# Kernel tuning notes

Measured on AMD Instinct MI355X. Metric: run time of the kernel, lower is better.

Reference implementation:

```python
import jax, jax.numpy as jnp
import numpy as np

B, T_ENC, T_DEC = 16, 256, 200
E, ATT, PRE, H, MEL, LOC, K = 512, 128, 256, 1024, 80, 32, 31


def setup_inputs() -> dict:
    key = jax.random.key(0)
    ks = jax.random.split(key, 20)
    s = lambda k, shape: jax.random.normal(k, shape, jnp.float32) * 0.02
    return dict(
        encoder_output=jax.random.normal(ks[0], (B, T_ENC, E), jnp.float32),
        padded_mels=jax.random.normal(ks[1], (B, T_DEC, MEL), jnp.float32),
        enc_proj_w=s(ks[2], (ATT, E)),
        lstm_proj_w=s(ks[3], (ATT, H)),
        loc_conv_w=s(ks[4], (LOC, 1, K)),
        loc_conv_b=jnp.zeros((LOC,), jnp.float32),
        loc_dense_w=s(ks[5], (ATT, LOC)),
        loc_dense_b=jnp.zeros((ATT,), jnp.float32),
        e_w=s(ks[6], (1, ATT)),
        e_b=jnp.zeros((1,), jnp.float32),
        prenet1_w=s(ks[7], (PRE, MEL)),
        prenet2_w=s(ks[8], (PRE, PRE)),
        w_ih0=s(ks[9], (4 * H, PRE + E)),
        w_hh0=s(ks[10], (4 * H, H)),
        b_ih0=jnp.zeros((4 * H,), jnp.float32),
        b_hh0=jnp.zeros((4 * H,), jnp.float32),
        w_ih1=s(ks[11], (4 * H, H)),
        w_hh1=s(ks[12], (4 * H, H)),
        b_ih1=jnp.zeros((4 * H,), jnp.float32),
        b_hh1=jnp.zeros((4 * H,), jnp.float32),
        proj_w=s(ks[13], (MEL, H + E)),
        proj_b=jnp.zeros((MEL,), jnp.float32),
        stop_w=s(ks[14], (1, H + E)),
        stop_b=jnp.zeros((1,), jnp.float32),
        text_lengths=jax.random.randint(ks[15], (B,), T_ENC // 2, T_ENC + 1),
    )


def _lstm_cell_zero(x, w_ih, b_ih, b_hh):
    # PyTorch LSTM cell with zero initial (h, c): h_prev contributes nothing
    # except the recurrent bias b_hh. Gate order: i, f, g, o.
    g = x @ w_ih.T + b_ih + b_hh
    i, f, gg, o = jnp.split(g, 4, axis=-1)
    c = jax.nn.sigmoid(i) * jnp.tanh(gg)  # f * c_prev == 0
    return jax.nn.sigmoid(o) * jnp.tanh(c)


def reference(encoder_output, padded_mels, enc_proj_w, lstm_proj_w, loc_conv_w,
              loc_conv_b, loc_dense_w, loc_dense_b, e_w, e_b, prenet1_w,
              prenet2_w, w_ih0, w_hh0, b_ih0, b_hh0, w_ih1, w_hh1, b_ih1,
              b_hh1, proj_w, proj_b, stop_w, stop_b, text_lengths):
    b, t_enc, _ = encoder_output.shape
    n_mel = padded_mels.shape[-1]
    h = w_hh0.shape[-1]
    pad = (loc_conv_w.shape[-1] - 1) // 2
    proc_enc = encoder_output @ enc_proj_w.T              # [B,Te,128]
    mask = jnp.arange(t_enc)[None, :] < text_lengths[:, None]
    # teacher forcing (ratio=1.0): prev mel at step t is padded_mels[:, t-1]
    prev_mels = jnp.concatenate(
        [jnp.zeros((b, 1, n_mel), padded_mels.dtype), padded_mels[:, :-1]],
        axis=1).transpose(1, 0, 2)                        # [Td,B,80]

    def step(carry, prev_mel):
        awc, h2 = carry                                   # [B,Te], [B,1024]
        # prenet (dropout omitted for a deterministic reference)
        x = jax.nn.relu(prev_mel @ prenet1_w.T)
        x = jax.nn.relu(x @ prenet2_w.T)                  # [B,256]
        # location-sensitive attention
        q = h2 @ lstm_proj_w.T                            # [B,128]
        loc = jax.lax.conv_general_dilated(
            awc[:, None, :], loc_conv_w, (1,), [(pad, pad)],
            dimension_numbers=('NCH', 'OIH', 'NCH')) + loc_conv_b[None, :, None]
        loc = jnp.einsum('bct,ac->bta', loc, loc_dense_w) + loc_dense_b
        en = jnp.tanh(q[:, None, :] + loc + proc_enc) @ e_w[0] + e_b[0]
        en = jnp.where(mask, en, -1e9)
        aw = jax.nn.softmax(en, axis=-1)                  # [B,Te]
        ctx = jnp.einsum('bt,bte->be', aw, encoder_output)  # [B,512]
        # 2-layer LSTM, state reset to zero every step (as in the original)
        li = jnp.concatenate([x, ctx], axis=-1)           # [B,768]
        h1 = _lstm_cell_zero(li, w_ih0, b_ih0, b_hh0)
        h2n = _lstm_cell_zero(h1, w_ih1, b_ih1, b_hh1)
        dec = jnp.concatenate([h2n, ctx], axis=-1)        # [B,1536]
        mel = dec @ proj_w.T + proj_b                     # [B,80]
        stop = (dec @ stop_w.T + stop_b)[:, 0]            # [B]
        return (awc + aw, h2n), (mel, stop)

    init = (jnp.zeros((b, t_enc), encoder_output.dtype),
            jnp.zeros((b, h), encoder_output.dtype))
    _, (mels, stops) = jax.lax.scan(step, init, prev_mels)
    return mels.transpose(1, 0, 2), stops.T               # [B,Td,80], [B,Td]
```

## Files before the change

kernel.cpp:

```cpp
#include <hip/hip_runtime.h>
#include <math.h>

#define NB   16
#define TE   256
#define TD   200
#define EE   512
#define ATT  128
#define PREN 256
#define HH   1024
#define NMEL 80
#define NLOC 32
#define KWW  31
#define PADW 15

#define OFF_X2H  0
#define OFF_PE   (OFF_X2H + TD*NB*128)
#define OFF_EN   (OFF_PE + NB*TE*ATT)
#define OFF_CTH  (OFF_EN + NB*TE)
#define OFF_H1H  (OFF_CTH + NB*256)
#define OFF_H2R  (OFF_H1H + NB*512)
#define OFF_QVR  (OFF_H2R + NB*256*4)
#define OFF_BAR  (OFF_QVR + NB*16*2*4)
#define BAR_U32  8192
#define ARR_G 0
#define ARR_L 4096

#define LW0X_U32 (12*128)
#define LW0C_U32 (12*256)
#define LW1_U32  (12*512)
#define DYN_BYTES ((LW0X_U32 + LW0C_U32 + LW1_U32)*4)

typedef float f4 __attribute__((ext_vector_type(4)));
typedef unsigned int u32x4 __attribute__((ext_vector_type(4)));
typedef unsigned int u32x2 __attribute__((ext_vector_type(2)));
typedef _Float16 h2t __attribute__((ext_vector_type(2)));

__device__ __forceinline__ float sigmf(float x) { return 1.0f / (1.0f + expf(-x)); }
__device__ __forceinline__ float dot4(f4 a, f4 b) {
  return a.x*b.x + a.y*b.y + a.z*b.z + a.w*b.w;
}
__device__ __forceinline__ float red32(float v) {
  v += __shfl_down(v, 16, 32); v += __shfl_down(v, 8, 32);
  v += __shfl_down(v, 4, 32);  v += __shfl_down(v, 2, 32);
  v += __shfl_down(v, 1, 32);
  return v;
}
__device__ __forceinline__ float red64(float v) {
  v += __shfl_down(v, 32); v += __shfl_down(v, 16); v += __shfl_down(v, 8);
  v += __shfl_down(v, 4);  v += __shfl_down(v, 2);  v += __shfl_down(v, 1);
  return v;
}
__device__ __forceinline__ float fdot2(unsigned a, unsigned b, float c) {
  return __builtin_amdgcn_fdot2(__builtin_bit_cast(h2t, a),
                                __builtin_bit_cast(h2t, b), c, false);
}
__device__ __forceinline__ unsigned pkh(float a, float b) {
  h2t h; h.x = (_Float16)a; h.y = (_Float16)b;
  return __builtin_bit_cast(unsigned, h);
}
__device__ __forceinline__ float hlo(unsigned u) {
  return (float)__builtin_bit_cast(h2t, u).x;
}
__device__ __forceinline__ float hhi(unsigned u) {
  return (float)__builtin_bit_cast(h2t, u).y;
}

__device__ __forceinline__ unsigned ld_cg_u32(const unsigned* p) {
  unsigned r;
  asm volatile("global_load_dword %0, %1, off sc0 sc1\n\ts_waitcnt vmcnt(0)"
               : "=v"(r) : "v"(p) : "memory");
  return r;
}
__device__ __forceinline__ void st_cg_u32(unsigned* p, unsigned v) {
  asm volatile("global_store_dword %0, %1, off sc0 sc1" :: "v"(p), "v"(v) : "memory");
}
__device__ __forceinline__ float ld_cg_f32(const float* p) {
  float r;
  asm volatile("global_load_dword %0, %1, off sc0 sc1\n\ts_waitcnt vmcnt(0)"
               : "=v"(r) : "v"(p) : "memory");
  return r;
}
__device__ __forceinline__ void st_cg_f32(float* p, float v) {
  asm volatile("global_store_dword %0, %1, off sc0 sc1" :: "v"(p), "v"(v) : "memory");
}
__device__ __forceinline__ f4 ld_cg_f4(const f4* p) {
  f4 r;
  asm volatile("global_load_dwordx4 %0, %1, off sc0 sc1\n\ts_waitcnt vmcnt(0)"
               : "=v"(r) : "v"(p) : "memory");
  return r;
}
__device__ __forceinline__ void st_cg_f4(f4* p, f4 v) {
  asm volatile("global_store_dwordx4 %0, %1, off sc0 sc1" :: "v"(p), "v"(v) : "memory");
}
__device__ __forceinline__ u32x4 ld_cg_u4(const void* p) {
  u32x4 r;
  asm volatile("global_load_dwordx4 %0, %1, off sc0 sc1\n\ts_waitcnt vmcnt(0)"
               : "=v"(r) : "v"(p) : "memory");
  return r;
}
__device__ __forceinline__ void st_cg_u2(void* p, u32x2 v) {
  asm volatile("global_store_dwordx2 %0, %1, off sc0 sc1" :: "v"(p), "v"(v) : "memory");
}
__device__ __forceinline__ void ld2u(u32x4& a, u32x4& b, const void* pa, const void* pb) {
  asm volatile(
    "global_load_dwordx4 %0, %2, off sc0 sc1\n\t"
    "global_load_dwordx4 %1, %3, off sc0 sc1\n\t"
    "s_waitcnt vmcnt(0)"
    : "=&v"(a), "=&v"(b) : "v"(pa), "v"(pb) : "memory");
}
__device__ __forceinline__ void ld4u(u32x4& a, u32x4& b, u32x4& c, u32x4& d,
                                     const void* pa, const void* pb,
                                     const void* pc, const void* pd) {
  asm volatile(
    "global_load_dwordx4 %0, %4, off sc0 sc1\n\t"
    "global_load_dwordx4 %1, %5, off sc0 sc1\n\t"
    "global_load_dwordx4 %2, %6, off sc0 sc1\n\t"
    "global_load_dwordx4 %3, %7, off sc0 sc1\n\t"
    "s_waitcnt vmcnt(0)"
    : "=&v"(a), "=&v"(b), "=&v"(c), "=&v"(d)
    : "v"(pa), "v"(pb), "v"(pc), "v"(pd) : "memory");
}

__device__ __forceinline__ void g_arrive(unsigned* bar, unsigned e) {
  __syncthreads();
  if (threadIdx.x == 0) st_cg_u32(bar + ARR_G + blockIdx.x * 16, e);
}
__device__ __forceinline__ void g_wait(unsigned* bar, unsigned e) {
  if (threadIdx.x < 256) {
    while (ld_cg_u32(bar + ARR_G + threadIdx.x * 16) < e) {}
  }
  __syncthreads();
}
__device__ __forceinline__ void l_arrive(unsigned* bar, unsigned e) {
  __syncthreads();
  if (threadIdx.x == 0) st_cg_u32(bar + ARR_L + blockIdx.x * 16, e);
}
__device__ __forceinline__ void l_wait(unsigned* bar, unsigned e, int b_grp) {
  if (threadIdx.x < 16) {
    while (ld_cg_u32(bar + ARR_L + (threadIdx.x * 16 + b_grp) * 16) < e) {}
  }
  __syncthreads();
}

__global__ void k_init(float* __restrict__ ws) {
  const int gid = blockIdx.x * 256 + threadIdx.x;
  f4* h2r = (f4*)(ws + OFF_H2R);
  f4* qvr = (f4*)(ws + OFF_QVR);
  unsigned* bar = (unsigned*)(ws + OFF_BAR);
  const f4 z = (f4){0.f, 0.f, 0.f, 0.f};
  for (int i = gid; i < NB*256; i += 32*256) st_cg_f4(h2r + i, z);
  for (int i = gid; i < NB*16*2; i += 32*256) st_cg_f4(qvr + i, z);
  for (int i = gid; i < BAR_U32; i += 32*256) st_cg_u32(bar + i, 0u);
}

__global__ void k_prenet(const float* __restrict__ mels,
                         const float* __restrict__ w1,
                         const float* __restrict__ w2,
                         float* __restrict__ ws) {
  const int t = blockIdx.x >> 4;
  const int b = blockIdx.x & 15;
  const int j = threadIdx.x;
  __shared__ float s_in[NMEL];
  __shared__ float s_x1[PREN];
  if (j < NMEL) s_in[j] = (t == 0) ? 0.0f : mels[(b*TD + (t-1))*NMEL + j];
  __syncthreads();
  float a1 = 0.0f;
  #pragma unroll 8
  for (int k = 0; k < NMEL; ++k) a1 += s_in[k] * w1[j*NMEL + k];
  s_x1[j] = fmaxf(a1, 0.0f);
  __syncthreads();
  float a2 = 0.0f;
  #pragma unroll 8
  for (int k = 0; k < PREN; ++k) a2 += s_x1[k] * w2[j*PREN + k];
  ((_Float16*)(ws + OFF_X2H))[((size_t)t*NB + b)*256 + j] = (_Float16)fmaxf(a2, 0.0f);
}

__global__ void k_procenc(const float* __restrict__ enc,
                          const float* __restrict__ w,
                          float* __restrict__ pe) {
  const int bt = blockIdx.x;
  const int a = threadIdx.x;
  __shared__ float s_e[EE];
  for (int k = a; k < EE; k += 128) s_e[k] = enc[bt*EE + k];
  __syncthreads();
  float acc = 0.0f;
  #pragma unroll 8
  for (int k = 0; k < EE; ++k) acc += s_e[k] * w[a*EE + k];
  pe[bt*ATT + a] = acc;
}

__global__ void __launch_bounds__(512, 1) k_main(
    const float* __restrict__ enc,
    const float* __restrict__ lstm_proj_w,
    const float* __restrict__ loc_conv_w,
    const float* __restrict__ loc_conv_b,
    const float* __restrict__ loc_dense_w,
    const float* __restrict__ loc_dense_b,
    const float* __restrict__ e_w,
    const float* __restrict__ e_b,
    const float* __restrict__ w_ih0,
    const float* __restrict__ b_ih0,
    const float* __restrict__ b_hh0,
    const float* __restrict__ w_ih1,
    const float* __restrict__ b_ih1,
    const float* __restrict__ b_hh1,
    const float* __restrict__ proj_w,
    const float* __restrict__ proj_b,
    const float* __restrict__ stop_w,
    const float* __restrict__ stop_b,
    const int*   __restrict__ text_len,
    float* __restrict__ ws,
    float* __restrict__ out) {
  const int bid = blockIdx.x;
  const int tid = threadIdx.x;

  const unsigned* x2h = (const unsigned*)(ws + OFF_X2H);
  float* pe  = ws + OFF_PE;
  float* en  = ws + OFF_EN;
  unsigned* cth = (unsigned*)(ws + OFF_CTH);
  unsigned* h1h = (unsigned*)(ws + OFF_H1H);
  f4* h2_rec = (f4*)(ws + OFF_H2R);
  f4* qv_rec = (f4*)(ws + OFF_QVR);
  unsigned* bar = (unsigned*)(ws + OFF_BAR);

  __shared__ __align__(16) float s_ldw[NLOC*ATT];
  __shared__ float s_awcf[TE];
  __shared__ float s_loc[16*33];
  __shared__ float s_red[16];
  __shared__ float s_aw[256];
  __shared__ float s_qtmp[8];
  __shared__ float s_ctmp[32];
  __shared__ __align__(16) float s_q[ATT];
  __shared__ __align__(16) float s_dec[HH+EE];
  __shared__ float s_b0[12], s_b1[12];
  extern __shared__ __align__(16) unsigned dynlds_u[];
  unsigned* lw0x = dynlds_u;
  unsigned* lw0c = lw0x + LW0X_U32;
  unsigned* lw1  = lw0c + LW0C_U32;

  const int b_grp = bid & 15;
  const int sub   = bid >> 4;
  const int h0    = bid * 4;

  for (int i = tid; i < NLOC*ATT; i += 512) {
    int c = i >> 7, a = i & 127;
    s_ldw[i] = loc_dense_w[a*NLOC + c];
  }
  if (tid < 12) {
    int g = tid >> 2, h = tid & 3;
    int gr = (g == 0 ? 0 : (g == 1 ? 2048 : 3072)) + h0 + h;
    s_b0[tid] = b_ih0[gr] + b_hh0[gr];
    s_b1[tid] = b_ih1[gr] + b_hh1[gr];
  }
  for (int i = tid; i < LW0X_U32; i += 512) {
    int r = i >> 7, c = i & 127;
    int g = r >> 2, h = r & 3;
    int grow = (g == 0 ? 0 : (g == 1 ? 2048 : 3072)) + h0 + h;
    const float* wr = w_ih0 + (size_t)grow*768;
    lw0x[i] = pkh(wr[2*c], wr[2*c+1]);
  }
  for (int i = tid; i < LW0C_U32; i += 512) {
    int r = i >> 8, c = i & 255;
    int g = r >> 2, h = r & 3;
    int grow = (g == 0 ? 0 : (g == 1 ? 2048 : 3072)) + h0 + h;
    const float* wr = w_ih0 + (size_t)grow*768 + 256;
    lw0c[i] = pkh(wr[2*c], wr[2*c+1]);
  }
  for (int i = tid; i < LW1_U32; i += 512) {
    int r = i >> 9, c = i & 511;
    int g = r >> 2, h = r & 3;
    int grow = (g == 0 ? 0 : (g == 1 ? 2048 : 3072)) + h0 + h;
    const float* wr = w_ih1 + (size_t)grow*1024;
    lw1[i] = pkh(wr[2*c], wr[2*c+1]);
  }
  if (tid < 256) s_awcf[tid] = 0.0f;

  const int   lenb = text_len[b_grp];
  const float eb0  = e_b[0];
  const int tl = tid >> 5;
  const int j  = tid & 31;
  float lcw_r[KWW];
  #pragma unroll
  for (int k = 0; k < KWW; ++k) lcw_r[k] = loc_conv_w[j*KWW + k];
  const float lcb_r = loc_conv_b[j];
  const f4 db_r = *(const f4*)(loc_dense_b + 4*j);
  const f4 ew_r = *(const f4*)(e_w + 4*j);
  const f4 pe_r = *(const f4*)(pe + (size_t)(b_grp*TE + sub*16 + tl)*ATT + 4*j);
  const f4 ps_r = pe_r + db_r;
  const int e4i = tid >> 6;
  const int ts  = tid & 63;
  f4 encr[4];
  {
    const f4* enc4 = (const f4*)(enc + (size_t)b_grp*TE*EE);
    #pragma unroll
    for (int i = 0; i < 4; ++i)
      encr[i] = enc4[(size_t)(ts + 64*i)*(EE/4) + sub*8 + e4i];
  }
  const int pb = tid >> 5;
  const int kc = tid & 31;
  __syncthreads();

  unsigned eg = 0, el = 0;

  for (int t = 0; t < TD; ++t) {
    const unsigned tg = (unsigned)(t + 1);
    f4 pre;
    {
      float cv = lcb_r;
      const int pos = sub*16 + tl;
      #pragma unroll
      for (int k = 0; k < KWW; ++k) {
        const int g = pos - PADW + k;
        const float av = (g >= 0 && g < TE) ? s_awcf[g] : 0.0f;
        cv += av * lcw_r[k];
      }
      s_loc[tl*33 + j] = cv;
      __syncthreads();
      f4 d4 = (f4){0.f, 0.f, 0.f, 0.f};
      #pragma unroll 8
      for (int c = 0; c < NLOC; ++c) {
        const float lv = s_loc[tl*33 + c];
        const f4 w4 = ((const f4*)s_ldw)[c*32 + j];
        d4.x += lv*w4.x; d4.y += lv*w4.y; d4.z += lv*w4.z; d4.w += lv*w4.w;
      }
      pre = ps_r + d4;
    }
    {
      if (tid < 32) {
        const int src = tid >> 1, r = tid & 1;
        const f4* qp = qv_rec + (b_grp*16 + src)*2 + r;
        f4 v;
        do { v = ld_cg_f4(qp); } while (__float_as_uint(v.z) != (unsigned)t);
        const unsigned u0 = __float_as_uint(v.x), u1 = __float_as_uint(v.y);
        const int base = src*8 + r*4;
        s_q[base+0] = hlo(u0); s_q[base+1] = hhi(u0);
        s_q[base+2] = hlo(u1); s_q[base+3] = hhi(u1);
      }
      __syncthreads();
      const f4 q4 = *(const f4*)(s_q + 4*j);
      float acc = tanhf(pre.x+q4.x)*ew_r.x + tanhf(pre.y+q4.y)*ew_r.y
                + tanhf(pre.z+q4.z)*ew_r.z + tanhf(pre.w+q4.w)*ew_r.w;
      acc = red32(acc);
      if (j == 0) {
        float evv = acc + eb0;
        const int tt = sub*16 + tl;
        if (tt >= lenb) evv = -1e9f;
        st_cg_f32(en + b_grp*TE + tt, evv);
      }
    }
    l_arrive(bar, ++el);
    if (t > 0) {
      const int ol = tid >> 5, kq = tid & 31;
      if (ol < 6) {
        const int m = sub*6 + ol;
        if (m < 81) {
          const float* wrow = (m < NMEL) ? (proj_w + (size_t)m*(HH+EE)) : stop_w;
          const f4* w4 = (const f4*)wrow;
          const f4* s4 = (const f4*)s_dec;
          float a2 = 0.0f;
          #pragma unroll
          for (int i = 0; i < 12; ++i) a2 += dot4(s4[kq + 32*i], w4[kq + 32*i]);
          a2 = red32(a2);
          if (kq == 0) {
            if (m < NMEL) out[(b_grp*TD + (t-1))*NMEL + m] = a2 + proj_b[m];
            else          out[NB*TD*NMEL + b_grp*TD + (t-1)] = a2 + stop_b[0];
          }
        }
      }
    }
    l_wait(bar, el, b_grp);
    {
      float evv = 0.f, p = 0.f;
      if (tid < 256) {
        evv = ld_cg_f32(en + b_grp*TE + tid);
        float m = evv;
        #pragma unroll
        for (int d = 32; d > 0; d >>= 1) m = fmaxf(m, __shfl_xor(m, d));
        if ((tid & 63) == 0) s_red[tid >> 6] = m;
      }
      __syncthreads();
      const float mx = fmaxf(fmaxf(s_red[0], s_red[1]), fmaxf(s_red[2], s_red[3]));
      if (tid < 256) {
        p = expf(evv - mx);
        float sm = p;
        #pragma unroll
        for (int d = 32; d > 0; d >>= 1) sm += __shfl_xor(sm, d);
        if ((tid & 63) == 0) s_red[8 + (tid >> 6)] = sm;
      }
      __syncthreads();
      const float inv = 1.0f / (s_red[8] + s_red[9] + s_red[10] + s_red[11]);
      if (tid < 256) {
        const float aw = p * inv;
        s_aw[tid] = aw;
        s_awcf[tid] += aw;
      }
      __syncthreads();
      f4 a4 = (f4){0.f, 0.f, 0.f, 0.f};
      #pragma unroll
      for (int i = 0; i < 4; ++i) {
        const float awv = s_aw[ts + 64*i];
        a4.x += awv*encr[i].x; a4.y += awv*encr[i].y;
        a4.z += awv*encr[i].z; a4.w += awv*encr[i].w;
      }
      a4.x = red64(a4.x); a4.y = red64(a4.y); a4.z = red64(a4.z); a4.w = red64(a4.w);
      if (ts == 0) {
        s_ctmp[e4i*4+0] = a4.x; s_ctmp[e4i*4+1] = a4.y;
        s_ctmp[e4i*4+2] = a4.z; s_ctmp[e4i*4+3] = a4.w;
      }
      __syncthreads();
      if (tid < 4) {
        u32x4 w;
        w.x = pkh(s_ctmp[8*tid+0], s_ctmp[8*tid+1]);
        w.y = pkh(s_ctmp[8*tid+2], s_ctmp[8*tid+3]);
        w.z = pkh(s_ctmp[8*tid+4], s_ctmp[8*tid+5]);
        w.w = pkh(s_ctmp[8*tid+6], s_ctmp[8*tid+7]);
        u32x4* dst = (u32x4*)cth + b_grp*64 + sub*4 + tid;
        asm volatile("global_store_dwordx4 %0, %1, off sc0 sc1" :: "v"(dst), "v"(w) : "memory");
      }
    }
    g_arrive(bar, ++eg);
    float acc[12];
    {
      #pragma unroll
      for (int r = 0; r < 12; ++r) acc[r] = 0.0f;
      const u32x4 xv = ((const u32x4*)x2h)[((size_t)t*NB + pb)*32 + kc];
      #pragma unroll
      for (int r = 0; r < 12; ++r) {
        const u32x4 w = ((const u32x4*)lw0x)[r*32 + kc];
        acc[r] = fdot2(xv.x, w.x, acc[r]); acc[r] = fdot2(xv.y, w.y, acc[r]);
        acc[r] = fdot2(xv.z, w.z, acc[r]); acc[r] = fdot2(xv.w, w.w, acc[r]);
      }
    }
    g_wait(bar, eg);
    {
      u32x4 c0, c1;
      const u32x4* cp = (const u32x4*)cth + pb*64 + kc;
      ld2u(c0, c1, cp, cp + 32);
      #pragma unroll
      for (int r = 0; r < 12; ++r) {
        const u32x4 w0 = ((const u32x4*)lw0c)[r*64 + kc];
        const u32x4 w1 = ((const u32x4*)lw0c)[r*64 + kc + 32];
        acc[r] = fdot2(c0.x, w0.x, acc[r]); acc[r] = fdot2(c0.y, w0.y, acc[r]);
        acc[r] = fdot2(c0.z, w0.z, acc[r]); acc[r] = fdot2(c0.w, w0.w, acc[r]);
        acc[r] = fdot2(c1.x, w1.x, acc[r]); acc[r] = fdot2(c1.y, w1.y, acc[r]);
        acc[r] = fdot2(c1.z, w1.z, acc[r]); acc[r] = fdot2(c1.w, w1.w, acc[r]);
      }
      #pragma unroll
      for (int r = 0; r < 12; ++r) acc[r] = red32(acc[r]);
      if (kc == 0) {
        float hv[4];
        #pragma unroll
        for (int h = 0; h < 4; ++h) {
          const float gi = acc[h]   + s_b0[h];
          const float gg = acc[4+h] + s_b0[4+h];
          const float go = acc[8+h] + s_b0[8+h];
          hv[h] = sigmf(go) * tanhf(sigmf(gi) * tanhf(gg));
        }
        u32x2 stv; stv.x = pkh(hv[0], hv[1]); stv.y = pkh(hv[2], hv[3]);
        st_cg_u2((u32x2*)h1h + pb*256 + bid, stv);
      }
    }
    g_arrive(bar, ++eg);
    g_wait(bar, eg);
    {
      #pragma unroll
      for (int r = 0; r < 12; ++r) acc[r] = 0.0f;
      u32x4 v0, v1, v2, v3;
      const u32x4* hp = (const u32x4*)h1h + pb*128 + kc;
      ld4u(v0, v1, v2, v3, hp, hp+32, hp+64, hp+96);
      #pragma unroll
      for (int r = 0; r < 12; ++r) {
        const u32x4* wp = (const u32x4*)lw1 + r*128 + kc;
        const u32x4 w0 = wp[0], w1 = wp[32], w2 = wp[64], w3 = wp[96];
        acc[r] = fdot2(v0.x, w0.x, acc[r]); acc[r] = fdot2(v0.y, w0.y, acc[r]);
        acc[r] = fdot2(v0.z, w0.z, acc[r]); acc[r] = fdot2(v0.w, w0.w, acc[r]);
        acc[r] = fdot2(v1.x, w1.x, acc[r]); acc[r] = fdot2(v1.y, w1.y, acc[r]);
        acc[r] = fdot2(v1.z, w1.z, acc[r]); acc[r] = fdot2(v1.w, w1.w, acc[r]);
        acc[r] = fdot2(v2.x, w2.x, acc[r]); acc[r] = fdot2(v2.y, w2.y, acc[r]);
        acc[r] = fdot2(v2.z, w2.z, acc[r]); acc[r] = fdot2(v2.w, w2.w, acc[r]);
        acc[r] = fdot2(v3.x, w3.x, acc[r]); acc[r] = fdot2(v3.y, w3.y, acc[r]);
        acc[r] = fdot2(v3.z, w3.z, acc[r]); acc[r] = fdot2(v3.w, w3.w, acc[r]);
      }
      #pragma unroll
      for (int r = 0; r < 12; ++r) acc[r] = red32(acc[r]);
      if (kc == 0) {
        float hv[4];
        #pragma unroll
        for (int h = 0; h < 4; ++h) {
          const float gi = acc[h]   + s_b1[h];
          const float gg = acc[4+h] + s_b1[4+h];
          const float go = acc[8+h] + s_b1[8+h];
          hv[h] = sigmf(go) * tanhf(sigmf(gi) * tanhf(gg));
        }
        f4 r;
        r.x = __uint_as_float(pkh(hv[0], hv[1]));
        r.y = __uint_as_float(pkh(hv[2], hv[3]));
        r.z = __uint_as_float(tg); r.w = 0.f;
        st_cg_f4(h2_rec + pb*256 + bid, r);
      }
    }
    {
      if (tid < 256) {
        const f4* hp = h2_rec + b_grp*256 + tid;
        f4 v;
        do { v = ld_cg_f4(hp); } while (__float_as_uint(v.z) != tg);
        const unsigned u0 = __float_as_uint(v.x), u1 = __float_as_uint(v.y);
        s_dec[4*tid+0] = hlo(u0); s_dec[4*tid+1] = hhi(u0);
        s_dec[4*tid+2] = hlo(u1); s_dec[4*tid+3] = hhi(u1);
      } else if (tid < 320) {
        const int i = tid - 256;
        const u32x4 cv = ld_cg_u4((const u32x4*)cth + b_grp*64 + i);
        s_dec[HH + 8*i + 0] = hlo(cv.x); s_dec[HH + 8*i + 1] = hhi(cv.x);
        s_dec[HH + 8*i + 2] = hlo(cv.y); s_dec[HH + 8*i + 3] = hhi(cv.y);
        s_dec[HH + 8*i + 4] = hlo(cv.z); s_dec[HH + 8*i + 5] = hhi(cv.z);
        s_dec[HH + 8*i + 6] = hlo(cv.w); s_dec[HH + 8*i + 7] = hhi(cv.w);
      }
      __syncthreads();
      const int row = tid >> 6;
      const int kq  = tid & 63;
      const int a   = sub*8 + row;
      const f4* w4 = (const f4*)(lstm_proj_w + (size_t)a*HH);
      const f4* s4 = (const f4*)s_dec;
      float a2 = 0.0f;
      #pragma unroll
      for (int i = 0; i < 4; ++i) a2 += dot4(s4[kq + 64*i], w4[kq + 64*i]);
      a2 = red64(a2);
      if (kq == 0) s_qtmp[row] = a2;
      __syncthreads();
      if (tid < 2) {
        f4 r;
        r.x = __uint_as_float(pkh(s_qtmp[4*tid+0], s_qtmp[4*tid+1]));
        r.y = __uint_as_float(pkh(s_qtmp[4*tid+2], s_qtmp[4*tid+3]));
        r.z = __uint_as_float(tg); r.w = 0.f;
        st_cg_f4(qv_rec + (b_grp*16 + sub)*2 + tid, r);
      }
    }
  }
  __syncthreads();
  {
    const int ol = tid >> 5, kq = tid & 31;
    if (ol < 6) {
      const int m = sub*6 + ol;
      if (m < 81) {
        const float* wrow = (m < NMEL) ? (proj_w + (size_t)m*(HH+EE)) : stop_w;
        const f4* w4 = (const f4*)wrow;
        const f4* s4 = (const f4*)s_dec;
        float a2 = 0.0f;
        #pragma unroll
        for (int i = 0; i < 12; ++i) a2 += dot4(s4[kq + 32*i], w4[kq + 32*i]);
        a2 = red32(a2);
        if (kq == 0) {
          if (m < NMEL) out[(b_grp*TD + (TD-1))*NMEL + m] = a2 + proj_b[m];
          else          out[NB*TD*NMEL + b_grp*TD + (TD-1)] = a2 + stop_b[0];
        }
      }
    }
  }
}

extern "C" void kernel_launch(void* const* d_in, const int* in_sizes, int n_in,
                              void* d_out, int out_size, void* d_ws, size_t ws_size,
                              hipStream_t stream) {
  (void)in_sizes; (void)n_in; (void)out_size; (void)ws_size;
  const float* enc         = (const float*)d_in[0];
  const float* mels        = (const float*)d_in[1];
  const float* enc_proj_w  = (const float*)d_in[2];
  const float* lstm_proj_w = (const float*)d_in[3];
  const float* loc_conv_w  = (const float*)d_in[4];
  const float* loc_conv_b  = (const float*)d_in[5];
  const float* loc_dense_w = (const float*)d_in[6];
  const float* loc_dense_b = (const float*)d_in[7];
  const float* e_w         = (const float*)d_in[8];
  const float* e_b         = (const float*)d_in[9];
  const float* prenet1_w   = (const float*)d_in[10];
  const float* prenet2_w   = (const float*)d_in[11];
  const float* w_ih0       = (const float*)d_in[12];
  const float* b_ih0       = (const float*)d_in[14];
  const float* b_hh0       = (const float*)d_in[15];
  const float* w_ih1       = (const float*)d_in[16];
  const float* b_ih1       = (const float*)d_in[18];
  const float* b_hh1       = (const float*)d_in[19];
  const float* proj_w      = (const float*)d_in[20];
  const float* proj_b      = (const float*)d_in[21];
  const float* stop_w      = (const float*)d_in[22];
  const float* stop_b      = (const float*)d_in[23];
  const int*   text_len    = (const int*)d_in[24];
  float* ws  = (float*)d_ws;
  float* out = (float*)d_out;

  static int attr_set = 0;
  if (!attr_set) {
    hipFuncSetAttribute((const void*)k_main,
                        hipFuncAttributeMaxDynamicSharedMemorySize, DYN_BYTES);
    attr_set = 1;
  }

  k_init<<<dim3(32), dim3(256), 0, stream>>>(ws);
  k_prenet<<<dim3(TD*NB), dim3(256), 0, stream>>>(mels, prenet1_w, prenet2_w, ws);
  k_procenc<<<dim3(NB*TE), dim3(128), 0, stream>>>(enc, enc_proj_w, ws + OFF_PE);

  k_main<<<dim3(256), dim3(512), DYN_BYTES, stream>>>(
      enc, lstm_proj_w, loc_conv_w, loc_conv_b, loc_dense_w, loc_dense_b,
      e_w, e_b, w_ih0, b_ih0, b_hh0, w_ih1, b_ih1, b_hh1,
      proj_w, proj_b, stop_w, stop_b, text_len, ws, out);
}
```

Before: 3.934 ms.

## Replace local and global barriers with tagged per-record flags for energies and context

Drops the per-batch-group local barrier and one grid-wide barrier from each decoder step. Attention energies and context vectors are now written as records that carry the step tag, and consumers spin until every record they need holds the current tag. The aim is to cut barrier round-trips across all 256 blocks per step so blocks wait only on the data they actually read. In exchange, records are fatter (fewer useful bytes per store, more polling loads), and correctness now depends on the tag field being written atomically with its data.

```diff
diff --git a/kernel.cpp b/kernel.cpp
--- a/kernel.cpp
+++ b/kernel.cpp
@@ -15,15 +15,14 @@
 
 #define OFF_X2H  0
 #define OFF_PE   (OFF_X2H + TD*NB*128)
-#define OFF_EN   (OFF_PE + NB*TE*ATT)
-#define OFF_CTH  (OFF_EN + NB*TE)
-#define OFF_H1H  (OFF_CTH + NB*256)
+#define OFF_ENR  (OFF_PE + NB*TE*ATT)
+#define OFF_CTR  (OFF_ENR + NB*16*6*4)
+#define OFF_H1H  (OFF_CTR + NB*128*4)
 #define OFF_H2R  (OFF_H1H + NB*512)
 #define OFF_QVR  (OFF_H2R + NB*256*4)
 #define OFF_BAR  (OFF_QVR + NB*16*2*4)
-#define BAR_U32  8192
+#define BAR_U32  4096
 #define ARR_G 0
-#define ARR_L 4096
 
 #define LW0X_U32 (12*128)
 #define LW0C_U32 (12*256)
@@ -74,15 +73,6 @@
 __device__ __forceinline__ void st_cg_u32(unsigned* p, unsigned v) {
   asm volatile("global_store_dword %0, %1, off sc0 sc1" :: "v"(p), "v"(v) : "memory");
 }
-__device__ __forceinline__ float ld_cg_f32(const float* p) {
-  float r;
-  asm volatile("global_load_dword %0, %1, off sc0 sc1\n\ts_waitcnt vmcnt(0)"
-               : "=v"(r) : "v"(p) : "memory");
-  return r;
-}
-__device__ __forceinline__ void st_cg_f32(float* p, float v) {
-  asm volatile("global_store_dword %0, %1, off sc0 sc1" :: "v"(p), "v"(v) : "memory");
-}
 __device__ __forceinline__ f4 ld_cg_f4(const f4* p) {
   f4 r;
   asm volatile("global_load_dwordx4 %0, %1, off sc0 sc1\n\ts_waitcnt vmcnt(0)"
@@ -98,15 +88,11 @@
                : "=v"(r) : "v"(p) : "memory");
   return r;
 }
+__device__ __forceinline__ void st_cg_u4(void* p, u32x4 v) {
+  asm volatile("global_store_dwordx4 %0, %1, off sc0 sc1" :: "v"(p), "v"(v) : "memory");
+}
 __device__ __forceinline__ void st_cg_u2(void* p, u32x2 v) {
   asm volatile("global_store_dwordx2 %0, %1, off sc0 sc1" :: "v"(p), "v"(v) : "memory");
-}
-__device__ __forceinline__ void ld2u(u32x4& a, u32x4& b, const void* pa, const void* pb) {
-  asm volatile(
-    "global_load_dwordx4 %0, %2, off sc0 sc1\n\t"
-    "global_load_dwordx4 %1, %3, off sc0 sc1\n\t"
-    "s_waitcnt vmcnt(0)"
-    : "=&v"(a), "=&v"(b) : "v"(pa), "v"(pb) : "memory");
 }
 __device__ __forceinline__ void ld4u(u32x4& a, u32x4& b, u32x4& c, u32x4& d,
                                      const void* pa, const void* pb,
@@ -131,25 +117,20 @@
   }
   __syncthreads();
 }
-__device__ __forceinline__ void l_arrive(unsigned* bar, unsigned e) {
-  __syncthreads();
-  if (threadIdx.x == 0) st_cg_u32(bar + ARR_L + blockIdx.x * 16, e);
-}
-__device__ __forceinline__ void l_wait(unsigned* bar, unsigned e, int b_grp) {
-  if (threadIdx.x < 16) {
-    while (ld_cg_u32(bar + ARR_L + (threadIdx.x * 16 + b_grp) * 16) < e) {}
-  }
-  __syncthreads();
-}
 
 __global__ void k_init(float* __restrict__ ws) {
   const int gid = blockIdx.x * 256 + threadIdx.x;
+  f4* enr = (f4*)(ws + OFF_ENR);
+  u32x4* ctr = (u32x4*)(ws + OFF_CTR);
   f4* h2r = (f4*)(ws + OFF_H2R);
   f4* qvr = (f4*)(ws + OFF_QVR);
   unsigned* bar = (unsigned*)(ws + OFF_BAR);
   const f4 z = (f4){0.f, 0.f, 0.f, 0.f};
+  const u32x4 zu = (u32x4){0u, 0u, 0u, 0u};
+  for (int i = gid; i < NB*16*6; i += 32*256) st_cg_f4(enr + i, z);
+  for (int i = gid; i < NB*128; i += 32*256) st_cg_u4(ctr + i, zu);
   for (int i = gid; i < NB*256; i += 32*256) st_cg_f4(h2r + i, z);
-  for (int i = gid; i < NB*16*2; i += 32*256) st_cg_f4(qvr + i, z);
+  for (int i = gid; i < NB*32; i += 32*256) st_cg_f4(qvr + i, z);
   for (int i = gid; i < BAR_U32; i += 32*256) st_cg_u32(bar + i, 0u);
 }
 
@@ -216,8 +197,8 @@
 
   const unsigned* x2h = (const unsigned*)(ws + OFF_X2H);
   float* pe  = ws + OFF_PE;
-  float* en  = ws + OFF_EN;
-  unsigned* cth = (unsigned*)(ws + OFF_CTH);
+  f4* en_rec = (f4*)(ws + OFF_ENR);
+  u32x4* ct_rec = (u32x4*)(ws + OFF_CTR);
   unsigned* h1h = (unsigned*)(ws + OFF_H1H);
   f4* h2_rec = (f4*)(ws + OFF_H2R);
   f4* qv_rec = (f4*)(ws + OFF_QVR);
@@ -227,7 +208,9 @@
   __shared__ float s_awcf[TE];
   __shared__ float s_loc[16*33];
   __shared__ float s_red[16];
+  __shared__ float s_en[256];
   __shared__ float s_aw[256];
+  __shared__ float s_entmp[16];
   __shared__ float s_qtmp[8];
   __shared__ float s_ctmp[32];
   __shared__ __align__(16) float s_q[ATT];
@@ -296,11 +279,15 @@
     for (int i = 0; i < 4; ++i)
       encr[i] = enc4[(size_t)(ts + 64*i)*(EE/4) + sub*8 + e4i];
   }
+  const int en_si = tid / 6;
+  const int en_rr = tid - en_si*6;
+  const f4* en_myrec = en_rec + (b_grp*16 + en_si)*6 + en_rr;
   const int pb = tid >> 5;
   const int kc = tid & 31;
+  const u32x4* ct_my = ct_rec + pb*128;
   __syncthreads();
 
-  unsigned eg = 0, el = 0;
+  unsigned eg = 0;
 
   for (int t = 0; t < TD; ++t) {
     const unsigned tg = (unsigned)(t + 1);
@@ -345,13 +332,28 @@
         float evv = acc + eb0;
         const int tt = sub*16 + tl;
         if (tt >= lenb) evv = -1e9f;
-        st_cg_f32(en + b_grp*TE + tt, evv);
-      }
-    }
-    l_arrive(bar, ++el);
-    if (t > 0) {
-      const int ol = tid >> 5, kq = tid & 31;
-      if (ol < 6) {
+        s_entmp[tl] = evv;
+      }
+      __syncthreads();
+      if (tid < 6) {
+        f4 r = (f4){0.f, 0.f, 0.f, __uint_as_float(tg)};
+        const int base = 3*tid;
+        r.x = s_entmp[base];
+        if (base + 1 < 16) r.y = s_entmp[base+1];
+        if (base + 2 < 16) r.z = s_entmp[base+2];
+        st_cg_f4(en_rec + (b_grp*16 + sub)*6 + tid, r);
+      }
+    }
+    {
+      if (tid < 96) {
+        f4 v;
+        do { v = ld_cg_f4(en_myrec); } while (__float_as_uint(v.w) != tg);
+        const int base = en_si*16 + 3*en_rr;
+        s_en[base] = v.x;
+        if (3*en_rr + 1 < 16) s_en[base+1] = v.y;
+        if (3*en_rr + 2 < 16) s_en[base+2] = v.z;
+      } else if (t > 0 && tid >= 128 && tid < 320) {
+        const int ol = (tid - 128) >> 5, kq = tid & 31;
         const int m = sub*6 + ol;
         if (m < 81) {
           const float* wrow = (m < NMEL) ? (proj_w + (size_t)m*(HH+EE)) : stop_w;
@@ -367,12 +369,10 @@
           }
         }
       }
-    }
-    l_wait(bar, el, b_grp);
-    {
+      __syncthreads();
       float evv = 0.f, p = 0.f;
       if (tid < 256) {
-        evv = ld_cg_f32(en + b_grp*TE + tid);
+        evv = s_en[tid];
         float m = evv;
         #pragma unroll
         for (int d = 32; d > 0; d >>= 1) m = fmaxf(m, __shfl_xor(m, d));
@@ -408,17 +408,14 @@
         s_ctmp[e4i*4+2] = a4.z; s_ctmp[e4i*4+3] = a4.w;
       }
       __syncthreads();
-      if (tid < 4) {
+      if (tid < 8) {
         u32x4 w;
-        w.x = pkh(s_ctmp[8*tid+0], s_ctmp[8*tid+1]);
-        w.y = pkh(s_ctmp[8*tid+2], s_ctmp[8*tid+3]);
-        w.z = pkh(s_ctmp[8*tid+4], s_ctmp[8*tid+5]);
-        w.w = pkh(s_ctmp[8*tid+6], s_ctmp[8*tid+7]);
-        u32x4* dst = (u32x4*)cth + b_grp*64 + sub*4 + tid;
-        asm volatile("global_store_dwordx4 %0, %1, off sc0 sc1" :: "v"(dst), "v"(w) : "memory");
-      }
-    }
-    g_arrive(bar, ++eg);
+        w.x = pkh(s_ctmp[4*tid+0], s_ctmp[4*tid+1]);
+        w.y = pkh(s_ctmp[4*tid+2], s_ctmp[4*tid+3]);
+        w.z = tg; w.w = 0u;
+        st_cg_u4(ct_rec + b_grp*128 + sub*8 + tid, w);
+      }
+    }
     float acc[12];
     {
       #pragma unroll
@@ -431,11 +428,16 @@
         acc[r] = fdot2(xv.z, w.z, acc[r]); acc[r] = fdot2(xv.w, w.w, acc[r]);
       }
     }
-    g_wait(bar, eg);
     {
-      u32x4 c0, c1;
-      const u32x4* cp = (const u32x4*)cth + pb*64 + kc;
-      ld2u(c0, c1, cp, cp + 32);
+      u32x4 ra, rb, rc, rd;
+      for (;;) {
+        ld4u(ra, rb, rc, rd, ct_my + 2*kc, ct_my + 2*kc + 1,
+             ct_my + 2*kc + 64, ct_my + 2*kc + 65);
+        if (ra.z == tg && rb.z == tg && rc.z == tg && rd.z == tg) break;
+        __builtin_amdgcn_s_sleep(1);
+      }
+      const u32x4 c0 = (u32x4){ra.x, ra.y, rb.x, rb.y};
+      const u32x4 c1 = (u32x4){rc.x, rc.y, rd.x, rd.y};
       #pragma unroll
       for (int r = 0; r < 12; ++r) {
         const u32x4 w0 = ((const u32x4*)lw0c)[r*64 + kc];
@@ -507,13 +509,13 @@
         const unsigned u0 = __float_as_uint(v.x), u1 = __float_as_uint(v.y);
         s_dec[4*tid+0] = hlo(u0); s_dec[4*tid+1] = hhi(u0);
         s_dec[4*tid+2] = hlo(u1); s_dec[4*tid+3] = hhi(u1);
-      } else if (tid < 320) {
+      } else if (tid < 384) {
         const int i = tid - 256;
-        const u32x4 cv = ld_cg_u4((const u32x4*)cth + b_grp*64 + i);
-        s_dec[HH + 8*i + 0] = hlo(cv.x); s_dec[HH + 8*i + 1] = hhi(cv.x);
-        s_dec[HH + 8*i + 2] = hlo(cv.y); s_dec[HH + 8*i + 3] = hhi(cv.y);
-        s_dec[HH + 8*i + 4] = hlo(cv.z); s_dec[HH + 8*i + 5] = hhi(cv.z);
-        s_dec[HH + 8*i + 6] = hlo(cv.w); s_dec[HH + 8*i + 7] = hhi(cv.w);
+        const u32x4* cp = ct_rec + b_grp*128 + i;
+        u32x4 v;
+        do { v = ld_cg_u4(cp); } while (v.z != tg);
+        s_dec[HH + 4*i + 0] = hlo(v.x); s_dec[HH + 4*i + 1] = hhi(v.x);
+        s_dec[HH + 4*i + 2] = hlo(v.y); s_dec[HH + 4*i + 3] = hhi(v.y);
       }
       __syncthreads();
       const int row = tid >> 6;
```

Result: no change. 3.991 ms (+1.4%).
